# Performance work log

Measured on AMD Instinct MI355X. Metric: run time of the kernel, lower is better.

## Reference

```python
import jax, jax.numpy as jnp
import numpy as np
from jax import lax

H = 384
W = 384
N = H * W                 # flattened pixel count
N_LOC = N // 2            # unknown pixels with 3x3 matting-Laplacian stencils
KCM = 20                  # color-mixture KNN size
K_IU = 5                  # intra-unknown KNN size
NNZ_CM = N_LOC * KCM


def setup_inputs() -> dict:
    key = jax.random.key(0)
    ks = jax.random.split(key, 16)
    f32 = jnp.float32
    i32 = jnp.int32
    inp = {}
    inp["CM_weights"] = jax.random.uniform(ks[0], (N,), f32)
    inp["LOC_weights"] = jax.random.uniform(ks[1], (N,), f32)
    inp["IU_weights"] = jax.random.uniform(ks[2], (N,), f32)
    inp["KU_weights"] = jax.random.uniform(ks[3], (N,), f32)
    inp["lmbda"] = jnp.full((1,), 100.0, f32)
    inp["kToUconf"] = jax.random.uniform(ks[4], (N,), f32)
    inp["known"] = jax.random.uniform(ks[5], (N,), f32)
    inp["kToU"] = jax.random.uniform(ks[6], (N,), f32)
    inp["Wcm_data"] = jax.random.uniform(ks[7], (NNZ_CM,), f32)
    inp["LOC_flows"] = jax.random.uniform(ks[8], (9, 9, N_LOC), f32)
    inp["IU_flows"] = jax.random.uniform(ks[9], (N_LOC, K_IU), f32)
    inp["Wcm_row"] = jax.random.randint(ks[10], (NNZ_CM,), 0, N, dtype=i32)
    inp["Wcm_col"] = jax.random.randint(ks[11], (NNZ_CM,), 0, N, dtype=i32)
    # interior pixels so all 9 stencil neighbours are valid
    inp["LOC_inInd"] = jax.random.randint(ks[12], (N_LOC,), W + 1, N - W - 1, dtype=i32)
    inp["IU_inInd"] = jax.random.randint(ks[13], (N_LOC,), 0, N, dtype=i32)
    inp["IU_neighInd"] = jax.random.randint(ks[14], (N_LOC, K_IU), 0, N, dtype=i32)
    inp["width"] = W
    inp["cg_steps"] = 30
    return inp


def reference(CM_weights, LOC_weights, IU_weights, KU_weights, lmbda,
              kToUconf, known, kToU, Wcm_data, LOC_flows, IU_flows,
              Wcm_row, Wcm_col, LOC_inInd, IU_inInd, IU_neighInd,
              width, cg_steps):
    n = kToU.shape[0]
    seg = lambda v, i: jax.ops.segment_sum(v, i, num_segments=n)

    # --- color mixture: Wcm scaled by diag(CM_weights); L = diag(rowsum) - Wcm; Lcm = L^T L
    cm_vals = CM_weights[Wcm_row] * Wcm_data
    rs_cm = seg(cm_vals, Wcm_row)

    # --- matting Laplacian: 9x9 flows per unknown pixel over 3x3 stencil
    offs = jnp.array([-1 - width, -1, -1 + width, -width, 0, width,
                      1 - width, 1, 1 + width], dtype=LOC_inInd.dtype)
    neigh = LOC_inInd[:, None] + offs[None, :]                    # [n_loc, 9]
    fl = LOC_flows * LOC_weights[LOC_inInd][None, None, :]        # [9, 9, n_loc]
    nloc = neigh.shape[0]
    # entry (row=neigh[k,i], col=neigh[k,j]) has value fl[j, i, k]
    vals_m = jnp.transpose(fl, (2, 1, 0)).reshape(-1)
    rows_m = jnp.broadcast_to(neigh[:, :, None], (nloc, 9, 9)).reshape(-1)
    cols_m = jnp.broadcast_to(neigh[:, None, :], (nloc, 9, 9)).reshape(-1)
    rows_ms = jnp.concatenate([rows_m, cols_m])
    cols_ms = jnp.concatenate([cols_m, rows_m])
    vals_ms = 0.5 * jnp.concatenate([vals_m, vals_m])             # W = 0.5 (W + W^T)
    rs_m = seg(vals_ms, rows_ms)

    # --- intra-unknowns KNN affinities
    fiu = IU_flows * IU_weights[IU_inInd][:, None]                # [n_iu, K]
    rows_c0 = jnp.broadcast_to(IU_inInd[:, None], IU_neighInd.shape).reshape(-1)
    cols_c0 = IU_neighInd.reshape(-1)
    rows_cs = jnp.concatenate([rows_c0, cols_c0])
    cols_cs = jnp.concatenate([cols_c0, rows_c0])
    vals_cs = 0.5 * jnp.concatenate([fiu.reshape(-1), fiu.reshape(-1)])
    rs_c = seg(vals_cs, rows_cs)

    # --- diagonal data terms: KU + lmbda*known
    diag_ku = KU_weights * kToUconf + lmbda[0] * known
    b = diag_ku * kToU

    def matvec(v):
        # Lcm @ v = L^T (L v), keeping L in factored COO form
        Lv = rs_cm * v - seg(cm_vals * v[Wcm_col], Wcm_row)
        lcm = rs_cm * Lv - seg(cm_vals * Lv[Wcm_row], Wcm_col)
        lm = rs_m * v - seg(vals_ms * v[cols_ms], rows_ms)
        lc = rs_c * v - seg(vals_cs * v[cols_cs], rows_cs)
        return lcm + lm + lc + diag_ku * v

    def cg_step(carry, _):
        x, r, p, rs = carry
        Ap = matvec(p)
        alpha = rs / jnp.vdot(p, Ap)
        x = x + alpha * p
        r = r - alpha * Ap
        rs_new = jnp.vdot(r, r)
        p = r + (rs_new / rs) * p
        return (x, r, p, rs_new), None

    x0 = jnp.zeros_like(b)  # x0 = 0 as in MattingSolver
    (x, _, _, _), _ = lax.scan(cg_step, (x0, b, b, jnp.vdot(b, b)), None, length=cg_steps)
    return x
```

## Files before the change

kernel.cpp:

```cpp
#include <hip/hip_runtime.h>


#define TPB 256

__device__ __forceinline__ float blockReduce256(float v) {
  #pragma unroll
  for (int o = 32; o > 0; o >>= 1) v += __shfl_down(v, o, 64);
  __shared__ float s[4];
  int lane = threadIdx.x & 63, wv = threadIdx.x >> 6;
  if (lane == 0) s[wv] = v;
  __syncthreads();
  return (threadIdx.x == 0) ? (s[0] + s[1] + s[2] + s[3]) : 0.f;
}

__global__ void k_init0(const float* __restrict__ KUw, const float* __restrict__ kToUconf,
                        const float* __restrict__ lmbda, const float* __restrict__ known,
                        const float* __restrict__ kToU,
                        float* __restrict__ diag_ku, float2* __restrict__ PR,
                        float* __restrict__ x,
                        int* __restrict__ CNT, float* __restrict__ scal, int N)
{
  int i = blockIdx.x * TPB + threadIdx.x;
  if (i < 80) scal[i] = 0.f;
  if (i < 4 * N) CNT[i] = 0;
  float red = 0.f;
  if (i < N) {
    float dk = KUw[i] * kToUconf[i] + lmbda[0] * known[i];
    diag_ku[i] = dk;
    float b = dk * kToU[i];
    PR[i] = make_float2(b, b);
    x[i] = 0.f;
    red = b * b;
  }
  float v = blockReduce256(red);
  if (threadIdx.x == 0) atomicAdd(&scal[0], v);
}

__global__ void k_prep(float* __restrict__ LOC_flows, const int* __restrict__ LOC_inInd,
                       const float* __restrict__ LOCw, int NLOC)
{
  int k = blockIdx.x * TPB + threadIdx.x;
  float Fl[81];
  #pragma unroll
  for (int m = 0; m < 81; ++m) Fl[m] = LOC_flows[(size_t)m * NLOC + k];
  float hw = 0.5f * LOCw[LOC_inInd[k]];
  int idx = 0;
  #pragma unroll
  for (int a = 0; a < 9; ++a)
    #pragma unroll
    for (int b = a + 1; b < 9; ++b) {
      LOC_flows[(size_t)idx * NLOC + k] = hw * (Fl[a * 9 + b] + Fl[b * 9 + a]);
      ++idx;
    }
}

__global__ void k_sh(const int* __restrict__ LOC_inInd, int* __restrict__ CNT,
                     unsigned short* __restrict__ sTick, int N, int NLOC)
{
  int k = blockIdx.x * TPB + threadIdx.x;
  sTick[k] = (unsigned short)atomicAdd(&CNT[3 * N + LOC_inInd[k]], 1);
}

__global__ void k_wminit(int* __restrict__ CNT, const int* __restrict__ width_p, int N)
{
  int j = blockIdx.x * TPB + threadIdx.x;
  int wd = *width_p;
  const int offs[9] = {-1 - wd, -1, -1 + wd, -wd, 0, wd, 1 - wd, 1, 1 + wd};
  int s = 0;
  #pragma unroll
  for (int a = 0; a < 9; ++a) {
    int v = j - offs[a];
    if (v >= 0 && v < N) s += CNT[3 * N + v];
  }
  CNT[2 * N + j] = s;
}

__global__ void k_hist(const int* __restrict__ IU_inInd, const int* __restrict__ IU_neighInd,
                       int* __restrict__ CNT, unsigned short* __restrict__ tU,
                       int NLOC, int N)
{
  int k = blockIdx.x * TPB + threadIdx.x;
  tU[5 * NLOC + k] = (unsigned short)atomicAdd(&CNT[2 * N + IU_inInd[k]], 1);
  #pragma unroll
  for (int j = 0; j < 5; ++j)
    tU[j * NLOC + k] =
        (unsigned short)atomicAdd(&CNT[2 * N + IU_neighInd[k * 5 + j]], 1);
}

__global__ void k_scan1(int* __restrict__ OFF, int* __restrict__ bsum, int tot)
{
  __shared__ int s[TPB];
  int gid = blockIdx.x * TPB + threadIdx.x;
  int v = (gid < tot) ? OFF[gid] : 0;
  s[threadIdx.x] = v;
  __syncthreads();
  #pragma unroll
  for (int o = 1; o < TPB; o <<= 1) {
    int t = (threadIdx.x >= o) ? s[threadIdx.x - o] : 0;
    __syncthreads();
    s[threadIdx.x] += t;
    __syncthreads();
  }
  if (gid < tot) OFF[gid] = s[threadIdx.x] - v;
  if (threadIdx.x == TPB - 1) bsum[blockIdx.x] = s[threadIdx.x];
}

__global__ void k_scan2(int* __restrict__ bsum, int nPerArr)
{
  __shared__ int s[1024];
  int base = blockIdx.x * nPerArr;
  int v = (threadIdx.x < nPerArr) ? bsum[base + threadIdx.x] : 0;
  s[threadIdx.x] = v;
  __syncthreads();
  for (int o = 1; o < 1024; o <<= 1) {
    int t = (threadIdx.x >= o) ? s[threadIdx.x - o] : 0;
    __syncthreads();
    s[threadIdx.x] += t;
    __syncthreads();
  }
  if (threadIdx.x < nPerArr) bsum[base + threadIdx.x] = s[threadIdx.x] - v;
}

__global__ void k_scan3(int* __restrict__ OFF, const int* __restrict__ bsum, int tot)
{
  int gid = blockIdx.x * TPB + threadIdx.x;
  if (gid < tot) OFF[gid] += bsum[blockIdx.x];
}

__global__ void k_sc(const int* __restrict__ LOC_inInd, const int* __restrict__ OFF,
                     const unsigned short* __restrict__ sTick,
                     int* __restrict__ perm, int* __restrict__ LOC_inIndP,
                     int N, int NLOC)
{
  int k = blockIdx.x * TPB + threadIdx.x;
  int v = LOC_inInd[k];
  int pos = OFF[3 * N + v] + sTick[k];
  perm[pos] = k;
  LOC_inIndP[pos] = v;
}

__global__ void k_permS2(float* __restrict__ LOC_flows, const int* __restrict__ perm,
                         int NLOC)
{
  int kp = blockIdx.x * TPB + threadIdx.x;
  int k = perm[kp];
  #pragma unroll
  for (int m = 0; m < 36; ++m)
    LOC_flows[(size_t)(36 + m) * NLOC + kp] = LOC_flows[(size_t)m * NLOC + k];
}

__global__ void kA_cnt(const int* __restrict__ Wrow, const int* __restrict__ Wcol,
                       int* __restrict__ blockCnt, int NB1)
{
  __shared__ int h[1152];
  for (int m = threadIdx.x; m < 1152; m += TPB) h[m] = 0;
  __syncthreads();
  int base = blockIdx.x * 4096;
  #pragma unroll
  for (int m = 0; m < 16; ++m) {
    int e = base + m * TPB + threadIdx.x;
    atomicAdd(&h[Wrow[e] >> 8], 1);
    atomicAdd(&h[576 + (Wcol[e] >> 8)], 1);
  }
  __syncthreads();
  for (int m = threadIdx.x; m < 1152; m += TPB)
    blockCnt[m * NB1 + blockIdx.x] = h[m];
}

__global__ void kC_scatter(const float* __restrict__ CMw, const float* __restrict__ Wcm_data,
                           const int* __restrict__ Wrow, const int* __restrict__ Wcol,
                           const int* __restrict__ blockCnt,
                           int2* __restrict__ csrPk, int2* __restrict__ cscPk,
                           unsigned short* __restrict__ bRowR,
                           unsigned short* __restrict__ bRowC,
                           int NNZ, int NB1)
{
  __shared__ int cnt[1152];
  for (int m = threadIdx.x; m < 1152; m += TPB) cnt[m] = 0;
  __syncthreads();
  int base = blockIdx.x * 4096;
  #pragma unroll
  for (int m = 0; m < 16; ++m) {
    int e = base + m * TPB + threadIdx.x;
    int row = Wrow[e], col = Wcol[e];
    int cv = __float_as_int(CMw[row] * Wcm_data[e]);
    int bR = row >> 8, bC = col >> 8;
    int rR = atomicAdd(&cnt[bR], 1);
    int rC = atomicAdd(&cnt[576 + bC], 1);
    int sR = blockCnt[bR * NB1 + blockIdx.x] + rR;
    int sC = blockCnt[(576 + bC) * NB1 + blockIdx.x] + rC - NNZ;
    csrPk[sR] = make_int2(col, cv);
    bRowR[sR] = (unsigned short)(row & 255);
    cscPk[sC] = make_int2(row, cv);
    bRowC[sC] = (unsigned short)(col & 255);
  }
}

__global__ void kD_fin(const int* __restrict__ blockCnt,
                       int2* __restrict__ csrPk, int2* __restrict__ cscPk,
                       const unsigned short* __restrict__ bRowR,
                       const unsigned short* __restrict__ bRowC,
                       int* __restrict__ OFF, int NNZ, int N, int NB1)
{
  __shared__ unsigned short rw[4096];
  __shared__ int2 en[4096];
  __shared__ int hist[256];
  __shared__ int sc[256];
  int blk = blockIdx.x;
  int side = blk / 576, b = blk % 576;
  const unsigned short* bRow = side ? bRowC : bRowR;
  int2* pk = side ? cscPk : csrPk;
  int segBase = blockCnt[(side * 576 + b) * NB1] - side * NNZ;
  int segEnd  = (b == 575) ? NNZ
                           : (blockCnt[(side * 576 + b + 1) * NB1] - side * NNZ);
  int len = segEnd - segBase;
  for (int m = threadIdx.x; m < len; m += TPB) {
    rw[m] = bRow[segBase + m];
    en[m] = pk[segBase + m];
  }
  hist[threadIdx.x] = 0;
  __syncthreads();
  for (int m = threadIdx.x; m < len; m += TPB) atomicAdd(&hist[rw[m]], 1);
  __syncthreads();
  int v = hist[threadIdx.x];
  sc[threadIdx.x] = v;
  __syncthreads();
  #pragma unroll
  for (int o = 1; o < 256; o <<= 1) {
    int t = (threadIdx.x >= o) ? sc[threadIdx.x - o] : 0;
    __syncthreads();
    sc[threadIdx.x] += t;
    __syncthreads();
  }
  int cumv = sc[threadIdx.x] - v;
  OFF[side * N + b * 256 + threadIdx.x] = segBase + cumv;
  hist[threadIdx.x] = cumv;
  __syncthreads();
  for (int m = threadIdx.x; m < len; m += TPB) {
    int pos = atomicAdd(&hist[rw[m]], 1);
    pk[segBase + pos] = en[m];
  }
}

__global__ void k_fill(const int* __restrict__ LOC_inIndP, const int* __restrict__ width_p,
                       const int* __restrict__ IU_inInd, const int* __restrict__ IU_neighInd,
                       const int* __restrict__ OFF,
                       const unsigned short* __restrict__ tU,
                       int* __restrict__ gU,
                       int NLOC, int N, int B0)
{
  int blk = blockIdx.x;
  if (blk < B0) {
    int kp = blk * TPB + threadIdx.x;
    int wd = *width_p;
    int base = LOC_inIndP[kp];
    const int* cum = OFF + 3 * N;
    int rank = kp - cum[base];
    int hh[5][5];
    #pragma unroll
    for (int dr = 0; dr < 5; ++dr) {
      int c[6];
      #pragma unroll
      for (int m = 0; m < 6; ++m) {
        int v = base + (dr - 2) * wd + (m - 2);
        c[m] = (v <= 0) ? 0 : ((v >= N) ? NLOC : cum[v]);
      }
      #pragma unroll
      for (int m = 0; m < 5; ++m) hh[dr][m] = c[m + 1] - c[m];
    }
    const int CAv[9] = {-1, -1, -1, 0, 0, 0, 1, 1, 1};
    const int RAv[9] = {-1, 0, 1, -1, 0, 1, -1, 0, 1};
    #pragma unroll
    for (int a = 0; a < 9; ++a) {
      int T = 0;
      #pragma unroll
      for (int ap = 0; ap < a; ++ap)
        T += hh[RAv[a] - RAv[ap] + 2][CAv[a] - CAv[ap] + 2];
      int j = base + CAv[a] + RAv[a] * wd;
      gU[OFF[2 * N + j] + T + rank] = a * NLOC + kp;
    }
  } else {
    int k = (blk - B0) * TPB + threadIdx.x;
    gU[OFF[2 * N + IU_inInd[k]] + tU[5 * NLOC + k]] = 14 * NLOC + k;
    #pragma unroll
    for (int j = 0; j < 5; ++j)
      gU[OFF[2 * N + IU_neighInd[k * 5 + j]] + tU[j * NLOC + k]] =
          (9 + j) * NLOC + k;
  }
}

__global__ void k_it1(const float2* __restrict__ PR,
                      const float* __restrict__ S2p, const int* __restrict__ LOC_inIndP,
                      const int* __restrict__ width_p,
                      const float* __restrict__ IU_flows, const int* __restrict__ IU_inInd,
                      const int* __restrict__ IU_neighInd, const float* __restrict__ IUw,
                      const float* __restrict__ diag_ku,
                      const int* __restrict__ OFF, const int2* __restrict__ csrPk,
                      float* __restrict__ u_all,
                      float* __restrict__ Lv, float* __restrict__ rs_cm,
                      const float* __restrict__ rsN, const float* __restrict__ rsO, int first,
                      float* __restrict__ pAp_t,
                      int NNZ, int NLOC, int N, int B0, int B1)
{
  int blk = blockIdx.x;
  float beta = first ? 0.f : rsN[0] / rsO[0];
  float red = 0.f;
  if (blk < B0) {
    int kp = blk * TPB + threadIdx.x;
    int wd = *width_p;
    int base = LOC_inIndP[kp];
    const int offs[9] = {-1 - wd, -1, -1 + wd, -wd, 0, wd, 1 - wd, 1, 1 + wd};
    float pv[9];
    #pragma unroll
    for (int a = 0; a < 9; ++a) {
      float2 pr = PR[base + offs[a]];
      pv[a] = __builtin_fmaf(beta, pr.x, pr.y);
    }
    float u[9] = {0.f, 0.f, 0.f, 0.f, 0.f, 0.f, 0.f, 0.f, 0.f};
    float qf = 0.f;
    int idx = 0;
    #pragma unroll
    for (int a = 0; a < 9; ++a)
      #pragma unroll
      for (int b = a + 1; b < 9; ++b) {
        float sv = S2p[(size_t)idx * NLOC + kp];
        ++idx;
        float d = pv[a] - pv[b];
        float t = sv * d;
        u[a] += t; u[b] -= t;
        qf += t * d;
      }
    #pragma unroll
    for (int a = 0; a < 9; ++a) u_all[a * NLOC + kp] = u[a];
    red = qf;
  } else if (blk < B1) {
    int k = (blk - B0) * TPB + threadIdx.x;
    int r0 = IU_inInd[k];
    float hw = 0.5f * IUw[r0];
    float2 prr = PR[r0];
    float pr = __builtin_fmaf(beta, prr.x, prr.y);
    int c[5]; float w[5];
    #pragma unroll
    for (int j = 0; j < 5; ++j) {
      c[j] = IU_neighInd[k * 5 + j];
      w[j] = hw * IU_flows[k * 5 + j];
    }
    float pc[5];
    #pragma unroll
    for (int j = 0; j < 5; ++j) {
      float2 pp = PR[c[j]];
      pc[j] = __builtin_fmaf(beta, pp.x, pp.y);
    }
    float qf = 0.f, asum = 0.f;
    #pragma unroll
    for (int j = 0; j < 5; ++j) {
      float d = pr - pc[j];
      float uA = w[j] * d;
      u_all[(9 + j) * NLOC + k] = -uA;
      asum += uA;
      qf += uA * d;
    }
    u_all[14 * NLOC + k] = asum;
    red = qf;
  } else {
    int i = (blk - B1) * TPB + threadIdx.x;
    float2 pri = PR[i];
    float pi = __builtin_fmaf(beta, pri.x, pri.y);
    int s = OFF[i];
    int e = (i == N - 1) ? NNZ : OFF[i + 1];
    float acc = 0.f, rs = 0.f;
    int q = s;
    for (; q + 8 <= e; q += 8) {
      int2 ed[8];
      #pragma unroll
      for (int m = 0; m < 8; ++m) ed[m] = csrPk[q + m];
      float g[8];
      #pragma unroll
      for (int m = 0; m < 8; ++m) {
        float2 pp = PR[ed[m].x];
        g[m] = __builtin_fmaf(beta, pp.x, pp.y);
      }
      #pragma unroll
      for (int m = 0; m < 8; ++m) {
        float cv = __int_as_float(ed[m].y);
        rs += cv;
        acc += cv * (pi - g[m]);
      }
    }
    for (; q + 4 <= e; q += 4) {
      int2 ed[4];
      #pragma unroll
      for (int m = 0; m < 4; ++m) ed[m] = csrPk[q + m];
      float g[4];
      #pragma unroll
      for (int m = 0; m < 4; ++m) {
        float2 pp = PR[ed[m].x];
        g[m] = __builtin_fmaf(beta, pp.x, pp.y);
      }
      #pragma unroll
      for (int m = 0; m < 4; ++m) {
        float cv = __int_as_float(ed[m].y);
        rs += cv;
        acc += cv * (pi - g[m]);
      }
    }
    for (; q < e; ++q) {
      int2 ed = csrPk[q];
      float cv = __int_as_float(ed.y);
      float2 pp = PR[ed.x];
      rs += cv;
      acc += cv * (pi - __builtin_fmaf(beta, pp.x, pp.y));
    }
    Lv[i] = acc;
    rs_cm[i] = rs;
    red = diag_ku[i] * pi * pi + acc * acc;
  }
  float v = blockReduce256(red);
  if (threadIdx.x == 0) atomicAdd(pAp_t, v);
}

__global__ void k_it2(float* __restrict__ x, float2* __restrict__ PR,
                      const float* __restrict__ Lv,
                      const float* __restrict__ rs_cm, const float* __restrict__ diag_ku,
                      const int* __restrict__ OFF,
                      const int2* __restrict__ cscPk,
                      const int* __restrict__ gU, const float* __restrict__ u_all,
                      const float* __restrict__ rs_t, const float* __restrict__ pAp_t,
                      const float* __restrict__ rsO, int first,
                      float* __restrict__ rs_t1,
                      int NNZ, int NLOC, int N)
{
  int i = blockIdx.x * TPB + threadIdx.x;
  float alpha = rs_t[0] / pAp_t[0];
  float beta = first ? 0.f : rs_t[0] / rsO[0];
  float tg = 0.f;
  {
    int s0 = OFF[2 * N + i];
    int e0 = (i == N - 1) ? 15 * NLOC : OFF[2 * N + i + 1];
    int q = s0;
    for (; q + 8 <= e0; q += 8) {
      int g[8];
      #pragma unroll
      for (int m = 0; m < 8; ++m) g[m] = gU[q + m];
      float u[8];
      #pragma unroll
      for (int m = 0; m < 8; ++m) u[m] = u_all[g[m]];
      #pragma unroll
      for (int m = 0; m < 8; ++m) tg += u[m];
    }
    for (; q + 4 <= e0; q += 4) {
      int g[4];
      #pragma unroll
      for (int m = 0; m < 4; ++m) g[m] = gU[q + m];
      float u[4];
      #pragma unroll
      for (int m = 0; m < 4; ++m) u[m] = u_all[g[m]];
      #pragma unroll
      for (int m = 0; m < 4; ++m) tg += u[m];
    }
    for (; q < e0; ++q) tg += u_all[gU[q]];
  }
  float sc = 0.f;
  {
    int s0 = OFF[N + i];
    int e0 = (i == N - 1) ? NNZ : OFF[N + i + 1];
    int q = s0;
    for (; q + 8 <= e0; q += 8) {
      int2 ed[8];
      #pragma unroll
      for (int m = 0; m < 8; ++m) ed[m] = cscPk[q + m];
      float l[8];
      #pragma unroll
      for (int m = 0; m < 8; ++m) l[m] = Lv[ed[m].x];
      #pragma unroll
      for (int m = 0; m < 8; ++m) sc += __int_as_float(ed[m].y) * l[m];
    }
    for (; q + 4 <= e0; q += 4) {
      int2 ed[4];
      #pragma unroll
      for (int m = 0; m < 4; ++m) ed[m] = cscPk[q + m];
      float l[4];
      #pragma unroll
      for (int m = 0; m < 4; ++m) l[m] = Lv[ed[m].x];
      #pragma unroll
      for (int m = 0; m < 4; ++m) sc += __int_as_float(ed[m].y) * l[m];
    }
    for (; q < e0; ++q) {
      int2 ed = cscPk[q];
      sc += __int_as_float(ed.y) * Lv[ed.x];
    }
  }
  float2 pri = PR[i];
  float pi = __builtin_fmaf(beta, pri.x, pri.y);
  float Ap = diag_ku[i] * pi + rs_cm[i] * Lv[i] - sc + tg;
  x[i] += alpha * pi;
  float rn = pri.y - alpha * Ap;
  PR[i] = make_float2(pi, rn);
  float v = blockReduce256(rn * rn);
  if (threadIdx.x == 0) atomicAdd(rs_t1, v);
}

extern "C" void kernel_launch(void* const* d_in, const int* in_sizes, int n_in,
                              void* d_out, int out_size, void* d_ws, size_t ws_size,
                              hipStream_t stream)
{
  const float* CMw       = (const float*)d_in[0];
  const float* LOCw      = (const float*)d_in[1];
  const float* IUw       = (const float*)d_in[2];
  const float* KUw       = (const float*)d_in[3];
  const float* lmbda     = (const float*)d_in[4];
  const float* kToUconf  = (const float*)d_in[5];
  const float* known     = (const float*)d_in[6];
  const float* kToU      = (const float*)d_in[7];
  const float* Wcm_data  = (const float*)d_in[8];
  float*       LOC_flows = (float*)d_in[9];
  const float* IU_flows  = (const float*)d_in[10];
  const int*   Wrow      = (const int*)d_in[11];
  const int*   Wcol      = (const int*)d_in[12];
  const int*   LOC_inInd = (const int*)d_in[13];
  const int*   IU_inInd  = (const int*)d_in[14];
  const int*   IU_neighInd = (const int*)d_in[15];
  const int*   width_p   = (const int*)d_in[16];
  const int CG_STEPS = 30;

  const int N    = in_sizes[0];
  const int NNZ  = in_sizes[8];
  const int NLOC = in_sizes[13];

  float* x       = (float*)d_out;
  float2* PR     = (float2*)d_ws;
  float* Lv      = (float*)(PR + (size_t)N);
  float* rs_cm   = Lv + N;
  float* diag_ku = rs_cm + N;
  int2*  csrPk   = (int2*)(diag_ku + N);
  int2*  cscPk   = csrPk + (size_t)NNZ;
  int*   gU      = (int*)(cscPk + (size_t)NNZ);
  int*   OFF     = gU + (size_t)15 * NLOC;
  unsigned short* tr = (unsigned short*)(OFF + (size_t)4 * N);
  unsigned short* tc = tr + (size_t)NNZ;
  unsigned short* tU = tc + (size_t)NNZ;
  float* u_all   = (float*)tr;
  int*   bsum    = (int*)(tU + (size_t)6 * NLOC);
  float* scal    = (float*)(bsum + 4 * (N / TPB));
  int*   perm    = (int*)(scal + 80);
  int*   LOC_inIndP = perm + NLOC;
  unsigned short* sTick = (unsigned short*)(LOC_inIndP + NLOC);
  int*   blockCnt = (int*)(sTick + (size_t)NLOC);

  const int Bn = N / TPB;
  const int Bl = NLOC / TPB;
  const int Z4 = 4 * Bn;
  const int NB1 = NNZ / 4096;
  const int SC  = 1152 * NB1;
  int* bsum1 = blockCnt + SC;
  int* bsum2 = bsum1 + (SC + TPB - 1) / TPB;
  const int SCB  = (SC + TPB - 1) / TPB;
  const int SCB2 = (SCB + TPB - 1) / TPB;

  k_init0<<<Z4, TPB, 0, stream>>>(KUw, kToUconf, lmbda, known, kToU,
                                  diag_ku, PR, x, OFF, scal, N);
  k_prep<<<Bl, TPB, 0, stream>>>(LOC_flows, LOC_inInd, LOCw, NLOC);
  k_sh<<<Bl, TPB, 0, stream>>>(LOC_inInd, OFF, sTick, N, NLOC);
  k_wminit<<<Bn, TPB, 0, stream>>>(OFF, width_p, N);
  k_hist<<<Bl, TPB, 0, stream>>>(IU_inInd, IU_neighInd, OFF, tU, NLOC, N);
  k_scan1<<<Z4, TPB, 0, stream>>>(OFF, bsum, 4 * N);
  k_scan2<<<4, 1024, 0, stream>>>(bsum, Bn);
  k_scan3<<<Z4, TPB, 0, stream>>>(OFF, bsum, 4 * N);
  k_sc<<<Bl, TPB, 0, stream>>>(LOC_inInd, OFF, sTick, perm, LOC_inIndP, N, NLOC);
  k_permS2<<<Bl, TPB, 0, stream>>>(LOC_flows, perm, NLOC);
  kA_cnt<<<NB1, TPB, 0, stream>>>(Wrow, Wcol, blockCnt, NB1);
  k_scan1<<<SCB, TPB, 0, stream>>>(blockCnt, bsum1, SC);
  k_scan1<<<SCB2, TPB, 0, stream>>>(bsum1, bsum2, SCB);
  k_scan2<<<1, 1024, 0, stream>>>(bsum2, SCB2);
  k_scan3<<<SCB2, TPB, 0, stream>>>(bsum1, bsum2, SCB);
  k_scan3<<<SCB, TPB, 0, stream>>>(blockCnt, bsum1, SC);
  kC_scatter<<<NB1, TPB, 0, stream>>>(CMw, Wcm_data, Wrow, Wcol, blockCnt,
                                      csrPk, cscPk, tr, tc, NNZ, NB1);
  kD_fin<<<1152, TPB, 0, stream>>>(blockCnt, csrPk, cscPk, tr, tc,
                                   OFF, NNZ, N, NB1);
  k_fill<<<2 * Bl, TPB, 0, stream>>>(LOC_inIndP, width_p, IU_inInd, IU_neighInd,
                                     OFF, tU, gU, NLOC, N, Bl);

  const float* S2p = LOC_flows + (size_t)36 * NLOC;
  for (int t = 0; t < CG_STEPS; ++t) {
    const float* rsN = scal + t;
    const float* rsO = scal + (t == 0 ? 0 : t - 1);
    k_it1<<<2 * Bl + Bn, TPB, 0, stream>>>(
        PR, S2p, LOC_inIndP, width_p,
        IU_flows, IU_inInd, IU_neighInd, IUw,
        diag_ku, OFF, csrPk, u_all, Lv, rs_cm,
        rsN, rsO, (t == 0) ? 1 : 0, scal + 40 + t,
        NNZ, NLOC, N, Bl, 2 * Bl);
    k_it2<<<Bn, TPB, 0, stream>>>(
        x, PR, Lv, rs_cm, diag_ku, OFF, cscPk, gU, u_all,
        rsN, scal + 40 + t, rsO, (t == 0) ? 1 : 0, scal + t + 1,
        NNZ, NLOC, N);
  }
}
```

Baseline: 1.755 ms.

## Pack low row bits into value mantissa and double edges per scatter block

The CSR/CSC build no longer writes separate 16-bit local-row arrays. The low 8 bits of the row or column index are stored in the low mantissa bits of the packed value and cleared again after the in-bucket sort. Each count and scatter block also handles twice as many edges, which halves the per-block histogram table and the prefix-scan work. The trade is that stored Wcm values lose their 8 low mantissa bits, which slightly perturbs CG numerics.

```diff
diff --git a/kernel.cpp b/kernel.cpp
--- a/kernel.cpp
+++ b/kernel.cpp
@@ -155,9 +155,9 @@
   __shared__ int h[1152];
   for (int m = threadIdx.x; m < 1152; m += TPB) h[m] = 0;
   __syncthreads();
-  int base = blockIdx.x * 4096;
-  #pragma unroll
-  for (int m = 0; m < 16; ++m) {
+  int base = blockIdx.x * 8192;
+  #pragma unroll 4
+  for (int m = 0; m < 32; ++m) {
     int e = base + m * TPB + threadIdx.x;
     atomicAdd(&h[Wrow[e] >> 8], 1);
     atomicAdd(&h[576 + (Wcol[e] >> 8)], 1);
@@ -171,35 +171,29 @@
                            const int* __restrict__ Wrow, const int* __restrict__ Wcol,
                            const int* __restrict__ blockCnt,
                            int2* __restrict__ csrPk, int2* __restrict__ cscPk,
-                           unsigned short* __restrict__ bRowR,
-                           unsigned short* __restrict__ bRowC,
                            int NNZ, int NB1)
 {
   __shared__ int cnt[1152];
   for (int m = threadIdx.x; m < 1152; m += TPB) cnt[m] = 0;
   __syncthreads();
-  int base = blockIdx.x * 4096;
-  #pragma unroll
-  for (int m = 0; m < 16; ++m) {
+  int base = blockIdx.x * 8192;
+  #pragma unroll 4
+  for (int m = 0; m < 32; ++m) {
     int e = base + m * TPB + threadIdx.x;
     int row = Wrow[e], col = Wcol[e];
-    int cv = __float_as_int(CMw[row] * Wcm_data[e]);
+    int cv = __float_as_int(CMw[row] * Wcm_data[e]) & 0xFFFFFF00;
     int bR = row >> 8, bC = col >> 8;
     int rR = atomicAdd(&cnt[bR], 1);
     int rC = atomicAdd(&cnt[576 + bC], 1);
     int sR = blockCnt[bR * NB1 + blockIdx.x] + rR;
     int sC = blockCnt[(576 + bC) * NB1 + blockIdx.x] + rC - NNZ;
-    csrPk[sR] = make_int2(col, cv);
-    bRowR[sR] = (unsigned short)(row & 255);
-    cscPk[sC] = make_int2(row, cv);
-    bRowC[sC] = (unsigned short)(col & 255);
+    csrPk[sR] = make_int2(col, cv | (row & 255));
+    cscPk[sC] = make_int2(row, cv | (col & 255));
   }
 }
 
 __global__ void kD_fin(const int* __restrict__ blockCnt,
                        int2* __restrict__ csrPk, int2* __restrict__ cscPk,
-                       const unsigned short* __restrict__ bRowR,
-                       const unsigned short* __restrict__ bRowC,
                        int* __restrict__ OFF, int NNZ, int N, int NB1)
 {
   __shared__ unsigned short rw[4096];
@@ -208,15 +202,15 @@
   __shared__ int sc[256];
   int blk = blockIdx.x;
   int side = blk / 576, b = blk % 576;
-  const unsigned short* bRow = side ? bRowC : bRowR;
   int2* pk = side ? cscPk : csrPk;
   int segBase = blockCnt[(side * 576 + b) * NB1] - side * NNZ;
   int segEnd  = (b == 575) ? NNZ
                            : (blockCnt[(side * 576 + b + 1) * NB1] - side * NNZ);
   int len = segEnd - segBase;
   for (int m = threadIdx.x; m < len; m += TPB) {
-    rw[m] = bRow[segBase + m];
-    en[m] = pk[segBase + m];
+    int2 v = pk[segBase + m];
+    en[m] = v;
+    rw[m] = (unsigned short)(v.y & 255);
   }
   hist[threadIdx.x] = 0;
   __syncthreads();
@@ -238,7 +232,8 @@
   __syncthreads();
   for (int m = threadIdx.x; m < len; m += TPB) {
     int pos = atomicAdd(&hist[rw[m]], 1);
-    pk[segBase + pos] = en[m];
+    int2 e = en[m];
+    pk[segBase + pos] = make_int2(e.x, e.y & 0xFFFFFF00);
   }
 }
 
@@ -550,12 +545,12 @@
   const int Bn = N / TPB;
   const int Bl = NLOC / TPB;
   const int Z4 = 4 * Bn;
-  const int NB1 = NNZ / 4096;
+  const int NB1 = NNZ / 8192;
   const int SC  = 1152 * NB1;
   int* bsum1 = blockCnt + SC;
-  int* bsum2 = bsum1 + (SC + TPB - 1) / TPB;
   const int SCB  = (SC + TPB - 1) / TPB;
   const int SCB2 = (SCB + TPB - 1) / TPB;
+  int* bsum2 = bsum1 + SCB;
 
   k_init0<<<Z4, TPB, 0, stream>>>(KUw, kToUconf, lmbda, known, kToU,
                                   diag_ku, PR, x, OFF, scal, N);
@@ -575,9 +570,8 @@
   k_scan3<<<SCB2, TPB, 0, stream>>>(bsum1, bsum2, SCB);
   k_scan3<<<SCB, TPB, 0, stream>>>(blockCnt, bsum1, SC);
   kC_scatter<<<NB1, TPB, 0, stream>>>(CMw, Wcm_data, Wrow, Wcol, blockCnt,
-                                      csrPk, cscPk, tr, tc, NNZ, NB1);
-  kD_fin<<<1152, TPB, 0, stream>>>(blockCnt, csrPk, cscPk, tr, tc,
-                                   OFF, NNZ, N, NB1);
+                                      csrPk, cscPk, NNZ, NB1);
+  kD_fin<<<1152, TPB, 0, stream>>>(blockCnt, csrPk, cscPk, OFF, NNZ, N, NB1);
   k_fill<<<2 * Bl, TPB, 0, stream>>>(LOC_inIndP, width_p, IU_inInd, IU_neighInd,
                                      OFF, tU, gU, NLOC, N, Bl);
 
```

Result: faster. 1.709 ms (-2.6%).
